# Performance work log

Measured on AMD Instinct MI355X. Metric: run time of the kernel, lower is better.

The kernel has to match this reference:

```python
import jax, jax.numpy as jnp
import numpy as np

HID = 768; HEADS = 12; DH = 64; W = 256  # one-sided window (attention_window=512)
L = 2; VOCAB = 50265; FFN = 3072; NLAB = 8921; B = 2; S = 4096
NEG = -1e9


def _ln(x, s, b):
    m = x.mean(-1, keepdims=True)
    v = ((x - m) ** 2).mean(-1, keepdims=True)
    return (x - m) * jax.lax.rsqrt(v + 1e-5) * s + b


def setup_inputs() -> dict:
    key = jax.random.key(0)
    ks = iter(jax.random.split(key, 64))
    def n(shape, sd=0.02):
        return jax.random.normal(next(ks), shape, jnp.float32) * sd
    inp = {
        'input_ids': jax.random.randint(next(ks), (B, S), 0, VOCAB, dtype=jnp.int32),
        'attention_mask': jnp.ones((B, S), jnp.int32),
        'word_emb': n((VOCAB, HID)), 'pos_emb': n((S, HID)),
        'emb_ln_s': jnp.ones((HID,), jnp.float32), 'emb_ln_b': jnp.zeros((HID,), jnp.float32),
        'Wq': n((L, HID, HID)), 'bq': jnp.zeros((L, HID), jnp.float32),
        'Wk': n((L, HID, HID)), 'bk': jnp.zeros((L, HID), jnp.float32),
        'Wv': n((L, HID, HID)), 'bv': jnp.zeros((L, HID), jnp.float32),
        'Wqg': n((L, HID, HID)), 'bqg': jnp.zeros((L, HID), jnp.float32),
        'Wkg': n((L, HID, HID)), 'bkg': jnp.zeros((L, HID), jnp.float32),
        'Wvg': n((L, HID, HID)), 'bvg': jnp.zeros((L, HID), jnp.float32),
        'Wo': n((L, HID, HID)), 'bo': jnp.zeros((L, HID), jnp.float32),
        'ln1_s': jnp.ones((L, HID), jnp.float32), 'ln1_b': jnp.zeros((L, HID), jnp.float32),
        'W1': n((L, HID, FFN)), 'b1': jnp.zeros((L, FFN), jnp.float32),
        'W2': n((L, FFN, HID)), 'b2': jnp.zeros((L, HID), jnp.float32),
        'ln2_s': jnp.ones((L, HID), jnp.float32), 'ln2_b': jnp.zeros((L, HID), jnp.float32),
        'head_W': n((HID, NLAB)), 'head_b': jnp.zeros((NLAB,), jnp.float32),
    }
    return inp


def _forward(input_ids, attention_mask, word_emb, pos_emb, emb_ln_s, emb_ln_b,
             Wq, bq, Wk, bk, Wv, bv, Wqg, bqg, Wkg, bkg, Wvg, bvg, Wo, bo,
             ln1_s, ln1_b, W1, b1, W2, b2, ln2_s, ln2_b, head_W, head_b):
    Bc, Sc = input_ids.shape
    nc = Sc // W
    scale = 1.0 / np.sqrt(DH).astype(np.float32)
    # embeddings
    x = word_emb[input_ids] + pos_emb[None, :Sc]
    x = _ln(x, emb_ln_s, emb_ln_b)
    # static band masks: query pos c*W+p, key pos (c-1)*W+kk in the 3-chunk layout
    p = jnp.arange(W)
    kk = jnp.arange(3 * W)
    rel = kk[None, :] - W - p[:, None]                     # [W,3W] key_pos - query_pos
    cpos = (jnp.arange(nc)[:, None, None] - 1) * W + kk[None, None, :]  # [nc,1,3W]
    valid = (cpos >= 0) & (cpos < Sc) & (cpos != 0) & (jnp.abs(rel)[None, :, :] <= W)  # [nc,W,3W]
    am_keys = attention_mask[:, jnp.clip(cpos, 0, Sc - 1)] > 0  # [B,nc,1,3W]
    band_mask = valid[None] & am_keys                        # [B,nc,W,3W]

    def split_heads(t):
        return t.reshape(Bc, Sc, HEADS, DH).transpose(0, 2, 1, 3)

    def chunk3(t):  # [B,H,S,D] -> [B,H,nc,3W,D] keys/values of chunks c-1,c,c+1
        tp = jnp.pad(t, ((0, 0), (0, 0), (W, W), (0, 0)))
        tr = tp.reshape(Bc, HEADS, nc + 2, W, DH)
        return jnp.concatenate([tr[:, :, :-2], tr[:, :, 1:-1], tr[:, :, 2:]], axis=3)

    for l in range(L):
        q = split_heads(x @ Wq[l] + bq[l])
        k = split_heads(x @ Wk[l] + bk[l])
        v = split_heads(x @ Wv[l] + bv[l])
        qg = split_heads(x @ Wqg[l] + bqg[l])
        kg = split_heads(x @ Wkg[l] + bkg[l])
        vg = split_heads(x @ Wvg[l] + bvg[l])
        # sliding-window banded scores
        qc = q.reshape(Bc, HEADS, nc, W, DH)
        kc = chunk3(k)
        vc = chunk3(v)
        sc = jnp.einsum('bhcqd,bhckd->bhcqk', qc, kc) * scale   # [B,H,nc,W,3W]
        sc = jnp.where(band_mask[:, None], sc, NEG)
        # extra column: every local query attends to the global (CLS) key
        g_col = jnp.einsum('bhsd,bhd->bhs', q, kg[:, :, 0]) * scale
        full = jnp.concatenate([g_col[..., None], sc.reshape(Bc, HEADS, Sc, 3 * W)], axis=-1)
        probs = jax.nn.softmax(full, axis=-1)
        p_g = probs[..., 0]
        p_b = probs[..., 1:].reshape(Bc, HEADS, nc, W, 3 * W)
        out = jnp.einsum('bhcqk,bhckd->bhcqd', p_b, vc).reshape(Bc, HEADS, Sc, DH)
        out = out + p_g[..., None] * vg[:, :, 0][:, :, None, :]
        # global (CLS) query: full attention over all tokens with global projections
        gs = jnp.einsum('bhd,bhsd->bhs', qg[:, :, 0], kg) * scale
        gs = jnp.where(attention_mask[:, None, :] > 0, gs, NEG)
        gp = jax.nn.softmax(gs, axis=-1)
        out0 = jnp.einsum('bhs,bhsd->bhd', gp, vg)
        out = out.at[:, :, 0, :].set(out0)
        # output proj + residual + LN, then FFN + residual + LN
        attn = out.transpose(0, 2, 1, 3).reshape(Bc, Sc, HID) @ Wo[l] + bo[l]
        x = _ln(x + attn, ln1_s[l], ln1_b[l])
        h = jax.nn.gelu(x @ W1[l] + b1[l], approximate=False) @ W2[l] + b2[l]
        x = _ln(x + h, ln2_s[l], ln2_b[l])
    # head on CLS token (dropout is identity in eval)
    return x[:, 0] @ head_W + head_b


def reference(input_ids, attention_mask, word_emb, pos_emb, emb_ln_s, emb_ln_b,
              Wq, bq, Wk, bk, Wv, bv, Wqg, bqg, Wkg, bkg, Wvg, bvg, Wo, bo,
              ln1_s, ln1_b, W1, b1, W2, b2, ln2_s, ln2_b, head_W, head_b):
    return _forward(input_ids, attention_mask, word_emb, pos_emb, emb_ln_s, emb_ln_b,
                    Wq, bq, Wk, bk, Wv, bv, Wqg, bqg, Wkg, bkg, Wvg, bvg, Wo, bo,
                    ln1_s, ln1_b, W1, b1, W2, b2, ln2_s, ln2_b, head_W, head_b)
```

## Files before the change

### kernel.cpp

```cpp
#include <hip/hip_runtime.h>
#include <hip/hip_bf16.h>
#include <math.h>

#define HIDN 768
#define NHEAD 12
#define DHEAD 64
#define WWIN 256
#define NCHUNK 16
#define NLAYER 2
#define FFND 3072
#define NLABEL 8921
#define NB 2
#define NS 4096
#define NBS (NB*NS)

#define QSTR 3840
#define OQ   0
#define OK_  768
#define OV   1536
#define OKG  2304
#define OVG  3072

typedef __attribute__((ext_vector_type(8))) short bf16x8;
typedef __attribute__((ext_vector_type(4))) float f32x4;

__device__ __forceinline__ float bf2f(unsigned short u){
  union { unsigned int i; float f; } v; v.i = ((unsigned int)u) << 16; return v.f;
}
__device__ __forceinline__ unsigned short f2bf(float f){
  __hip_bfloat16 h = __float2bfloat16(f);
  return *reinterpret_cast<unsigned short*>(&h);
}
__device__ __forceinline__ void unpack2(unsigned int u, float& a, float& b){
  union { unsigned int i; float f; } x, y;
  x.i = u << 16; y.i = u & 0xffff0000u; a = x.f; b = y.f;
}
__device__ __forceinline__ float gelu_f(float v){
  float x = v * 0.70710678118f;
  float ax = fabsf(x);
  float t = 1.0f / (1.0f + 0.3275911f*ax);
  float poly = ((((1.061405429f*t - 1.453152027f)*t + 1.421413741f)*t
                - 0.284496736f)*t + 0.254829592f)*t;
  float y = 1.0f - poly*__expf(-x*x);
  float er = copysignf(y, x);
  return 0.5f*v*(1.0f + er);
}
__device__ __forceinline__ void gld_lds16(const unsigned short* g, unsigned short* l){
  __builtin_amdgcn_global_load_lds((const __attribute__((address_space(1))) unsigned int*)g,
                                   (__attribute__((address_space(3))) unsigned int*)l, 16, 0, 0);
}

__device__ __forceinline__ int xcd_swz(int orig, int nwg){
  int q = nwg >> 3, r = nwg & 7;
  int x = orig & 7, lo = orig >> 3;
  return (x < r ? x*(q+1) : r*(q+1) + (x-r)*q) + lo;
}

#define DPP_ROR_F(x, N) __builtin_bit_cast(float, __builtin_amdgcn_update_dpp( \
    0, __builtin_bit_cast(int, (x)), 0x120 + (N), 0xf, 0xf, true))
__device__ __forceinline__ float rowmax16(float x){
  x = fmaxf(x, DPP_ROR_F(x, 1));
  x = fmaxf(x, DPP_ROR_F(x, 2));
  x = fmaxf(x, DPP_ROR_F(x, 4));
  x = fmaxf(x, DPP_ROR_F(x, 8));
  return x;
}
__device__ __forceinline__ float rowsum16(float x){
  x = x + DPP_ROR_F(x, 1);
  x = x + DPP_ROR_F(x, 2);
  x = x + DPP_ROR_F(x, 4);
  x = x + DPP_ROR_F(x, 8);
  return x;
}

__global__ __launch_bounds__(256) void embed_k(const int* __restrict__ ids,
    const float* __restrict__ we, const float* __restrict__ pe,
    float* __restrict__ y){
  int i = blockIdx.x*256 + threadIdx.x;
  int row = i / HIDN; int d = i - row*HIDN;
  int s = row & (NS-1);
  int id = ids[row];
  y[i] = we[(size_t)id*HIDN + d] + pe[(size_t)s*HIDN + d];
}

__global__ __launch_bounds__(256) void ln_k(const float* A, const float* R,
    const float* __restrict__ sc, const float* __restrict__ bi,
    float* X, unsigned short* XB){
  __shared__ float red[256];
  int row = blockIdx.x, t = threadIdx.x;
  size_t base = (size_t)row*HIDN;
  float v0 = A[base+t], v1 = A[base+t+256], v2 = A[base+t+512];
  if (R){ v0 += R[base+t]; v1 += R[base+t+256]; v2 += R[base+t+512]; }
  red[t] = v0+v1+v2; __syncthreads();
  for (int st=128; st>0; st>>=1){ if (t<st) red[t]+=red[t+st]; __syncthreads(); }
  float mean = red[0] * (1.0f/HIDN); __syncthreads();
  float d0=v0-mean, d1=v1-mean, d2=v2-mean;
  red[t] = d0*d0+d1*d1+d2*d2; __syncthreads();
  for (int st=128; st>0; st>>=1){ if (t<st) red[t]+=red[t+st]; __syncthreads(); }
  float rs = rsqrtf(red[0] * (1.0f/HIDN) + 1e-5f);
  float o0 = d0*rs*sc[t]     + bi[t];
  float o1 = d1*rs*sc[t+256] + bi[t+256];
  float o2 = d2*rs*sc[t+512] + bi[t+512];
  X[base+t]=o0; X[base+t+256]=o1; X[base+t+512]=o2;
  XB[base+t]=f2bf(o0); XB[base+t+256]=f2bf(o1); XB[base+t+512]=f2bf(o2);
}

__global__ __launch_bounds__(256) void transpose_k(const float* __restrict__ src,
    unsigned short* __restrict__ dst, int R, int C){
  __shared__ unsigned short tile[32][33];
  int ct = blockIdx.x*32, rt = blockIdx.y*32;
  int tx = threadIdx.x, ty = threadIdx.y;
  #pragma unroll
  for (int i=0;i<4;i++) tile[ty+i*8][tx] = f2bf(src[(size_t)(rt+ty+i*8)*C + ct + tx]);
  __syncthreads();
  #pragma unroll
  for (int i=0;i<4;i++) dst[(size_t)(ct+ty+i*8)*R + rt + tx] = tile[tx][ty+i*8];
}

__global__ __launch_bounds__(256) void pack_bias_k(const float* __restrict__ bq,
    const float* __restrict__ bk, const float* __restrict__ bv,
    const float* __restrict__ bkg, const float* __restrict__ bvg,
    float* __restrict__ out){
  int i = blockIdx.x*256 + threadIdx.x;
  int l = i / QSTR; int j = i - l*QSTR;
  int seg = j / HIDN, d = j - seg*HIDN;
  const float* src = (seg==0)?bq : (seg==1)?bk : (seg==2)?bv : (seg==3)?bkg : bvg;
  out[i] = src[l*HIDN + d];
}

template<int OUTF32, int GELU>
__global__ __launch_bounds__(256) void gemm128(const unsigned short* __restrict__ A,
    const unsigned short* __restrict__ BT, const float* __restrict__ bias,
    void* __restrict__ Cp, int M, int N, int K){
  __shared__ unsigned short As[128*64];
  __shared__ unsigned short Bs[128*64];
  const int tid = threadIdx.x;
  const int nwg = gridDim.x * gridDim.y;
  const int wg = xcd_swz(blockIdx.y * gridDim.x + blockIdx.x, nwg);
  const int m0 = (wg / gridDim.x) * 128, n0 = (wg % gridDim.x) * 128;
  const int lane = tid & 63, w = tid >> 6;
  const int n = lane & 15, quad = lane >> 4;
  const int wm = (w>>1)*64, wn = (w&1)*64;
  const int lr = lane >> 3, site = lane & 7;
  f32x4 acc[4][4] = {};
  for (int kb=0; kb<K; kb+=64){
    #pragma unroll
    for (int j=0;j<4;j++){
      int rbase = w*32 + j*8;
      int r = rbase + lr;
      int q = site ^ (r & 7);
      gld_lds16(A  + (size_t)(m0+r)*K + kb + q*8, &As[rbase*64]);
      gld_lds16(BT + (size_t)(n0+r)*K + kb + q*8, &Bs[rbase*64]);
    }
    __syncthreads();
    #pragma unroll
    for (int ks=0; ks<2; ks++){
      bf16x8 a[4], b[4];
      #pragma unroll
      for (int i=0;i<4;i++){
        int rm = wm + i*16 + n;
        a[i] = *(const bf16x8*)&As[rm*64 + (((ks*4+quad) ^ (rm&7))<<3)];
        int rn = wn + i*16 + n;
        b[i] = *(const bf16x8*)&Bs[rn*64 + (((ks*4+quad) ^ (rn&7))<<3)];
      }
      #pragma unroll
      for (int mi=0;mi<4;mi++)
      #pragma unroll
      for (int ni=0;ni<4;ni++)
        acc[mi][ni] = __builtin_amdgcn_mfma_f32_16x16x32_bf16(a[mi], b[ni], acc[mi][ni], 0,0,0);
    }
    __syncthreads();
  }
  #pragma unroll
  for (int mi=0; mi<4; mi++)
  #pragma unroll
  for (int ni=0; ni<4; ni++){
    int col = n0 + wn + ni*16 + n;
    float bsv = bias[col];
    #pragma unroll
    for (int rg=0; rg<4; rg++){
      int row = m0 + wm + mi*16 + quad*4 + rg;
      float v = acc[mi][ni][rg] + bsv;
      if (GELU) v = gelu_f(v);
      if (OUTF32) ((float*)Cp)[(size_t)row*N + col] = v;
      else ((unsigned short*)Cp)[(size_t)row*N + col] = f2bf(v);
    }
  }
}

template<int OUTF32, int GELU>
__global__ __launch_bounds__(512) void gemm256(const unsigned short* __restrict__ A,
    const unsigned short* __restrict__ BT, const float* __restrict__ bias,
    void* __restrict__ Cp, int M, int N, int K){
  __shared__ unsigned short AsB[2][256*64];
  __shared__ unsigned short BsB[2][256*64];
  const int tid = threadIdx.x;
  const int gx = gridDim.x;
  const int nwg = gx * gridDim.y;
  const int wg = xcd_swz(blockIdx.y*gx + blockIdx.x, nwg);
  const int m0 = (wg / gx) * 256, n0 = (wg % gx) * 256;
  const int lane = tid & 63, w = tid >> 6;
  const int n = lane & 15, quad = lane >> 4;
  const int wm = (w>>2)*128, wn = (w&3)*64;
  const int lr = lane >> 3, site = lane & 7;
  const int NK = K >> 6;
  f32x4 acc[8][4] = {};

  auto stage = [&](int b, int kb){
    #pragma unroll
    for (int j=0;j<4;j++){
      int rbase = w*32 + j*8;
      int r = rbase + lr;
      int q = site ^ (r & 7);
      gld_lds16(A  + (size_t)(m0+r)*K + kb + q*8, &AsB[b][rbase*64]);
      gld_lds16(BT + (size_t)(n0+r)*K + kb + q*8, &BsB[b][rbase*64]);
    }
  };

  stage(0, 0);
  asm volatile("s_waitcnt vmcnt(0)" ::: "memory");
  __builtin_amdgcn_s_barrier();

  int cur = 0;
  for (int kt=0; kt<NK; ++kt){
    if (kt+1 < NK) stage(cur^1, (kt+1)<<6);
    const unsigned short* As_ = AsB[cur];
    const unsigned short* Bs_ = BsB[cur];
    bf16x8 bfr[2][4];
    #pragma unroll
    for (int ks=0;ks<2;ks++)
    #pragma unroll
    for (int ni=0;ni<4;ni++){
      int rn = wn + ni*16 + n;
      bfr[ks][ni] = *(const bf16x8*)&Bs_[rn*64 + (((ks*4+quad) ^ (rn&7))<<3)];
    }
    #pragma unroll
    for (int mi=0;mi<8;mi++){
      int rm = wm + mi*16 + n;
      bf16x8 a0 = *(const bf16x8*)&As_[rm*64 + (((quad)     ^ (rm&7))<<3)];
      bf16x8 a1 = *(const bf16x8*)&As_[rm*64 + (((4+quad)   ^ (rm&7))<<3)];
      #pragma unroll
      for (int ni=0;ni<4;ni++)
        acc[mi][ni] = __builtin_amdgcn_mfma_f32_16x16x32_bf16(a0, bfr[0][ni], acc[mi][ni],0,0,0);
      #pragma unroll
      for (int ni=0;ni<4;ni++)
        acc[mi][ni] = __builtin_amdgcn_mfma_f32_16x16x32_bf16(a1, bfr[1][ni], acc[mi][ni],0,0,0);
    }
    if (kt+1 < NK){
      asm volatile("s_waitcnt vmcnt(0)" ::: "memory");
      __builtin_amdgcn_s_barrier();
    }
    cur ^= 1;
  }
  #pragma unroll
  for (int mi=0;mi<8;mi++)
  #pragma unroll
  for (int ni=0;ni<4;ni++){
    int col = n0 + wn + ni*16 + n;
    float bsv = bias[col];
    #pragma unroll
    for (int rg=0;rg<4;rg++){
      int row = m0 + wm + mi*16 + quad*4 + rg;
      float v = acc[mi][ni][rg] + bsv;
      if (GELU) v = gelu_f(v);
      if (OUTF32) ((float*)Cp)[(size_t)row*N + col] = v;
      else ((unsigned short*)Cp)[(size_t)row*N + col] = f2bf(v);
    }
  }
}

__global__ __launch_bounds__(256, 2) void band_attn_mfma(
    const unsigned short* __restrict__ qkv, const int* __restrict__ am,
    unsigned short* __restrict__ Out){
  __shared__ unsigned short Kt[64*72];
  __shared__ unsigned short Vt[64*72];
  __shared__ unsigned short Pbuf[4*64*72];
  __shared__ float mk[64];
  __shared__ unsigned short kgs[64];
  __shared__ unsigned short vgs[64];

  const int tid = threadIdx.x;
  const int bid = xcd_swz(blockIdx.x, gridDim.x);
  const int c = bid & (NCHUNK-1);
  const int h = (bid / NCHUNK) % NHEAD;
  const int b = bid / (NCHUNK*NHEAD);
  const int lane = tid & 63, w = tid >> 6;
  const int n = lane & 15, quad = lane >> 4;
  const int qbase = w * 64;
  unsigned short* Pw = Pbuf + w*64*72;

  if (tid < 8)       ((uint4*)kgs)[tid]   = ((const uint4*)(qkv + ((size_t)b*NS)*QSTR + OKG + h*DHEAD))[tid];
  else if (tid < 16) ((uint4*)vgs)[tid-8] = ((const uint4*)(qkv + ((size_t)b*NS)*QSTR + OVG + h*DHEAD))[tid-8];
  __syncthreads();

  bf16x8 aQ[4][2];
  #pragma unroll
  for (int mi=0; mi<4; mi++)
  #pragma unroll
  for (int ks=0; ks<2; ks++)
    aQ[mi][ks] = *(const bf16x8*)(qkv + ((size_t)(b*NS + c*WWIN + qbase + 16*mi + n))*QSTR
                                    + OQ + h*DHEAD + ks*32 + quad*8);

  f32x4 sacc[4] = {};
  #pragma unroll
  for (int ks=0; ks<2; ks++){
    bf16x8 bg = *(const bf16x8*)(kgs + ks*32 + quad*8);
    bf16x8 z8 = {};
    bg = (n == 0) ? bg : z8;
    #pragma unroll
    for (int mi=0; mi<4; mi++)
      sacc[mi] = __builtin_amdgcn_mfma_f32_16x16x32_bf16(aQ[mi][ks], bg, sacc[mi], 0,0,0);
  }
  float mst[4][4], lpt[4][4];
  f32x4 apv[4][4];
  float vgf[4];
  #pragma unroll
  for (int ni=0; ni<4; ni++) vgf[ni] = bf2f(vgs[16*ni + n]);
  #pragma unroll
  for (int mi=0; mi<4; mi++)
  #pragma unroll
  for (int rg=0; rg<4; rg++){
    float sg = __shfl(sacc[mi][rg], lane & 48);
    mst[mi][rg] = sg * 0.125f;
    lpt[mi][rg] = (n == 0) ? 1.0f : 0.0f;
  }
  #pragma unroll
  for (int mi=0; mi<4; mi++)
  #pragma unroll
  for (int ni=0; ni<4; ni++)
  #pragma unroll
  for (int rg=0; rg<4; rg++) apv[mi][ni][rg] = vgf[ni];

  for (int t=0; t<12; t++){
    __syncthreads();
    {
      int i = tid >> 2, d0 = (tid & 3) * 8;
      int kp = (c-1)*WWIN + t*64 + i;
      int kpc = min(max(kp, 0), NS-1);
      size_t gb = ((size_t)(b*NS + kpc))*QSTR + h*DHEAD;
      uint4 k0 = *(const uint4*)(qkv + gb + OK_ + d0);
      uint4 k1 = *(const uint4*)(qkv + gb + OK_ + d0 + 32);
      uint4 v0 = *(const uint4*)(qkv + gb + OV + d0);
      uint4 v1 = *(const uint4*)(qkv + gb + OV + d0 + 32);
      *(uint4*)(Kt + i*72 + d0) = k0;
      *(uint4*)(Kt + i*72 + d0 + 32) = k1;
      const unsigned short* s0 = (const unsigned short*)&v0;
      const unsigned short* s1 = (const unsigned short*)&v1;
      #pragma unroll
      for (int j=0;j<8;j++){
        Vt[(d0+j)*72 + i] = s0[j];
        Vt[(d0+32+j)*72 + i] = s1[j];
      }
      if ((tid & 3) == 0)
        mk[i] = (kp >= 1 && kp < NS && am[b*NS + kpc] > 0) ? 0.0f : -1e9f;
    }
    __syncthreads();

    float mkv[4];
    #pragma unroll
    for (int ni=0; ni<4; ni++) mkv[ni] = mk[16*ni + n];

    f32x4 accs[4][4] = {};
    #pragma unroll
    for (int ks=0; ks<2; ks++){
      bf16x8 bK[4];
      #pragma unroll
      for (int ni=0; ni<4; ni++)
        bK[ni] = *(const bf16x8*)(Kt + (16*ni + n)*72 + ks*32 + quad*8);
      #pragma unroll
      for (int mi=0; mi<4; mi++)
      #pragma unroll
      for (int ni=0; ni<4; ni++)
        accs[mi][ni] = __builtin_amdgcn_mfma_f32_16x16x32_bf16(aQ[mi][ks], bK[ni], accs[mi][ni], 0,0,0);
    }

    #pragma unroll
    for (int mi=0; mi<4; mi++){
      float sv[4][4];
      #pragma unroll
      for (int ni=0; ni<4; ni++)
      #pragma unroll
      for (int rg=0; rg<4; rg++){
        int kk = t*64 + 16*ni + n;
        int pr = qbase + 16*mi + quad*4 + rg;
        float s = accs[mi][ni][rg]*0.125f + mkv[ni];
        if ((unsigned)(kk - pr) > 512u) s = -1e9f;
        sv[ni][rg] = s;
      }
      #pragma unroll
      for (int rg=0; rg<4; rg++){
        float rm = fmaxf(fmaxf(sv[0][rg], sv[1][rg]), fmaxf(sv[2][rg], sv[3][rg]));
        rm = rowmax16(rm);
        float mold = mst[mi][rg];
        float mnew = fmaxf(mold, rm);
        float alpha = __expf(mold - mnew);
        mst[mi][rg] = mnew;
        float psum = 0.f;
        #pragma unroll
        for (int ni=0; ni<4; ni++){
          float pv = __expf(sv[ni][rg] - mnew);
          sv[ni][rg] = pv;
          psum += pv;
        }
        lpt[mi][rg] = lpt[mi][rg]*alpha + psum;
        #pragma unroll
        for (int ni=0; ni<4; ni++) apv[mi][ni][rg] *= alpha;
        int prow = 16*mi + quad*4 + rg;
        #pragma unroll
        for (int ni=0; ni<4; ni++)
          Pw[prow*72 + 16*ni + n] = f2bf(sv[ni][rg]);
      }
    }

    #pragma unroll
    for (int ks2=0; ks2<2; ks2++){
      bf16x8 aP[4], bV[4];
      #pragma unroll
      for (int mi=0; mi<4; mi++)
        aP[mi] = *(const bf16x8*)(Pw + (16*mi + n)*72 + ks2*32 + quad*8);
      #pragma unroll
      for (int ni=0; ni<4; ni++)
        bV[ni] = *(const bf16x8*)(Vt + (16*ni + n)*72 + ks2*32 + quad*8);
      #pragma unroll
      for (int mi=0; mi<4; mi++)
      #pragma unroll
      for (int ni=0; ni<4; ni++)
        apv[mi][ni] = __builtin_amdgcn_mfma_f32_16x16x32_bf16(aP[mi], bV[ni], apv[mi][ni], 0,0,0);
    }
  }

  #pragma unroll
  for (int mi=0; mi<4; mi++)
  #pragma unroll
  for (int rg=0; rg<4; rg++){
    float L = rowsum16(lpt[mi][rg]);
    float inv = 1.0f / L;
    int q = c*WWIN + qbase + 16*mi + quad*4 + rg;
    size_t ob = ((size_t)(b*NS + q))*HIDN + h*DHEAD;
    #pragma unroll
    for (int ni=0; ni<4; ni++)
      Out[ob + 16*ni + n] = f2bf(apv[mi][ni][rg] * inv);
  }
}

__global__ __launch_bounds__(128) void gattn_part(
    const unsigned short* __restrict__ QG0, const unsigned short* __restrict__ qkv,
    const int* __restrict__ am, float* __restrict__ part){
  __shared__ float qs[64];
  __shared__ float ps[128];
  __shared__ float red[128];
  int t = threadIdx.x;
  int cx = blockIdx.x, h = blockIdx.y, b = blockIdx.z;
  if (t < 32){
    float a, bb; unpack2(((const unsigned int*)(QG0 + (size_t)b*128*HIDN + h*DHEAD))[t], a, bb);
    qs[2*t]=a*0.125f; qs[2*t+1]=bb*0.125f;
  }
  __syncthreads();
  int kp = cx*128 + t;
  const unsigned int* kr = (const unsigned int*)(qkv + ((size_t)(b*NS+kp))*QSTR + OKG + h*DHEAD);
  float sv = 0.f;
  #pragma unroll
  for (int j=0;j<32;j++){ float a,bb; unpack2(kr[j],a,bb); sv += qs[2*j]*a + qs[2*j+1]*bb; }
  if (am[b*NS+kp] <= 0) sv = -1e9f;
  red[t] = sv; __syncthreads();
  for (int st=64; st>0; st>>=1){ if (t<st) red[t] = fmaxf(red[t], red[t+st]); __syncthreads(); }
  float M = red[0]; __syncthreads();
  float e = __expf(sv - M);
  ps[t] = e; red[t] = e; __syncthreads();
  for (int st=64; st>0; st>>=1){ if (t<st) red[t] += red[t+st]; __syncthreads(); }
  float L = red[0];
  float* po = part + ((size_t)((b*NHEAD+h)*32 + cx))*66;
  if (t==0){ po[0]=M; po[1]=L; }
  if (t < 64){
    float o = 0.f;
    #pragma unroll 4
    for (int i=0;i<128;i++)
      o += ps[i] * bf2f(qkv[((size_t)(b*NS + cx*128 + i))*QSTR + OVG + h*DHEAD + t]);
    po[2+t] = o;
  }
}

__global__ __launch_bounds__(64) void gattn_reduce(const float* __restrict__ part,
    unsigned short* __restrict__ Out){
  int bh = blockIdx.x;
  int b = bh / NHEAD, h = bh % NHEAD;
  int d = threadIdx.x;
  const float* pp = part + (size_t)bh*32*66;
  float M = -1e30f;
  for (int c2=0;c2<32;c2++) M = fmaxf(M, pp[c2*66]);
  float L = 0.f, o = 0.f;
  for (int c2=0;c2<32;c2++){
    float w = __expf(pp[c2*66] - M);
    L += pp[c2*66+1]*w;
    o += pp[c2*66+2+d]*w;
  }
  Out[((size_t)b*NS)*HIDN + h*DHEAD + d] = f2bf(o / L);
}

__global__ __launch_bounds__(256) void head_k(const float* __restrict__ X,
    const float* __restrict__ HW, const float* __restrict__ HB,
    float* __restrict__ Outp){
  __shared__ float red[256];
  __shared__ float xs[HIDN];
  int b = blockIdx.y;
  int base = blockIdx.x*64;
  int t = threadIdx.x;
  const float* x0 = X + (size_t)b*NS*HIDN;
  for (int i=t; i<HIDN; i+=256) xs[i] = x0[i];
  __syncthreads();
  int n = base + (t & 63);
  int dp = t >> 6;
  float a = 0.f;
  if (n < NLABEL){
    #pragma unroll 4
    for (int d=dp*192; d<dp*192+192; ++d)
      a += xs[d] * HW[(size_t)d*NLABEL + n];
  }
  red[t] = a; __syncthreads();
  if (t < 64 && n < NLABEL)
    Outp[(size_t)b*NLABEL + n] = red[t]+red[t+64]+red[t+128]+red[t+192] + HB[n];
}

extern "C" void kernel_launch(void* const* d_in, const int* in_sizes, int n_in,
                              void* d_out, int out_size, void* d_ws, size_t ws_size,
                              hipStream_t stream){
  (void)in_sizes; (void)n_in; (void)out_size; (void)ws_size;
  const int* ids = (const int*)d_in[0];
  const int* am  = (const int*)d_in[1];
  const float* we  = (const float*)d_in[2];
  const float* pe  = (const float*)d_in[3];
  const float* elns= (const float*)d_in[4];
  const float* elnb= (const float*)d_in[5];
  const float* Wq  = (const float*)d_in[6];
  const float* bq  = (const float*)d_in[7];
  const float* Wk  = (const float*)d_in[8];
  const float* bk  = (const float*)d_in[9];
  const float* Wv  = (const float*)d_in[10];
  const float* bv  = (const float*)d_in[11];
  const float* Wqg = (const float*)d_in[12];
  const float* bqg = (const float*)d_in[13];
  const float* Wkg = (const float*)d_in[14];
  const float* bkg = (const float*)d_in[15];
  const float* Wvg = (const float*)d_in[16];
  const float* bvg = (const float*)d_in[17];
  const float* Wo  = (const float*)d_in[18];
  const float* bo  = (const float*)d_in[19];
  const float* l1s = (const float*)d_in[20];
  const float* l1b = (const float*)d_in[21];
  const float* W1  = (const float*)d_in[22];
  const float* b1  = (const float*)d_in[23];
  const float* W2  = (const float*)d_in[24];
  const float* b2  = (const float*)d_in[25];
  const float* l2s = (const float*)d_in[26];
  const float* l2b = (const float*)d_in[27];
  const float* hW  = (const float*)d_in[28];
  const float* hB  = (const float*)d_in[29];

  char* ws = (char*)d_ws;
  float* x = (float*)ws;
  float* y = (float*)(ws + 25165824);
  unsigned short* xb   = (unsigned short*)(ws + 50331648);
  unsigned short* qkvb = (unsigned short*)(ws + 62914560);
  unsigned short* qg0b = (unsigned short*)(ws + 125829120);
  float* part = (float*)(ws + 126222336);
  unsigned short* ao   = (unsigned short*)(ws + 126425088);
  unsigned short* hbuf = (unsigned short*)(ws + 139008000);
  unsigned short* wt   = (unsigned short*)(ws + 189339648);
  float* bpack = (float*)(ws + 224729088);

  const size_t SQ = 589824;
  const size_t SW = 2359296;
  const size_t PERL = 7*SQ + 2*SW;

  auto tr = [&](const float* src, unsigned short* dst, int R, int C){
    dim3 g(C/32, R/32), blk(32, 8);
    transpose_k<<<g, blk, 0, stream>>>(src, dst, R, C);
  };
  for (int l=0; l<NLAYER; l++){
    unsigned short* base = wt + (size_t)l*PERL;
    tr(Wq  + (size_t)l*SQ, base + 0*SQ, 768, 768);
    tr(Wk  + (size_t)l*SQ, base + 1*SQ, 768, 768);
    tr(Wv  + (size_t)l*SQ, base + 2*SQ, 768, 768);
    tr(Wkg + (size_t)l*SQ, base + 3*SQ, 768, 768);
    tr(Wvg + (size_t)l*SQ, base + 4*SQ, 768, 768);
    tr(Wqg + (size_t)l*SQ, base + 5*SQ, 768, 768);
    tr(Wo  + (size_t)l*SQ, base + 6*SQ, 768, 768);
    tr(W1  + (size_t)l*SW, base + 7*SQ, 768, 3072);
    tr(W2  + (size_t)l*SW, base + 7*SQ + SW, 3072, 768);
  }
  pack_bias_k<<<(NLAYER*QSTR)/256, 256, 0, stream>>>(bq, bk, bv, bkg, bvg, bpack);

  embed_k<<<(NBS*HIDN)/256, 256, 0, stream>>>(ids, we, pe, y);
  ln_k<<<NBS, 256, 0, stream>>>(y, nullptr, elns, elnb, x, xb);

  for (int l=0; l<NLAYER; l++){
    unsigned short* base = wt + (size_t)l*PERL;
    gemm256<0,0><<<dim3(15,32), 512, 0, stream>>>(xb, base, bpack + (size_t)l*QSTR,
                                                  qkvb, NBS, QSTR, 768);
    for (int b=0; b<NB; b++)
      gemm128<0,0><<<dim3(6,1), 256, 0, stream>>>(xb + (size_t)b*NS*HIDN, base + 5*SQ,
                                                  bqg + l*768, qg0b + (size_t)b*128*HIDN,
                                                  128, 768, 768);
    band_attn_mfma<<<NB*NHEAD*NCHUNK, 256, 0, stream>>>(qkvb, am, ao);
    gattn_part<<<dim3(32, NHEAD, NB), 128, 0, stream>>>(qg0b, qkvb, am, part);
    gattn_reduce<<<NB*NHEAD, 64, 0, stream>>>(part, ao);
    gemm128<1,0><<<dim3(6,64), 256, 0, stream>>>(ao, base + 6*SQ, bo + l*768, y, NBS, 768, 768);
    ln_k<<<NBS, 256, 0, stream>>>(y, x, l1s + l*768, l1b + l*768, x, xb);
    gemm256<0,1><<<dim3(12,32), 512, 0, stream>>>(xb, base + 7*SQ, b1 + l*3072, hbuf, NBS, 3072, 768);
    gemm128<1,0><<<dim3(6,64), 256, 0, stream>>>(hbuf, base + 7*SQ + SW, b2 + l*768, y, NBS, 768, 3072);
    ln_k<<<NBS, 256, 0, stream>>>(y, x, l2s + l*768, l2b + l*768, x, xb);
  }

  head_k<<<dim3((NLABEL+63)/64, NB), 256, 0, stream>>>(x, hW, hB, (float*)d_out);
}
```

Baseline: 1.165 ms.

## Batch weight transposes into one launch, merge qg GEMMs, single-buffer gemm256

All 18 weight transpose launches are folded into one kernel that looks up its matrix from a block-offset table. The two per-batch global-query GEMM launches become one launch with a z-dimension. gemm256 drops its double-buffered LDS prefetch for a single buffer with __syncthreads and adds s_setprio around the MFMA loop. This cuts launch overhead and halves gemm256 LDS use, which may allow more occupancy, but it gives up overlap of global loads with compute in the largest GEMMs.

```diff
diff --git a/kernel.cpp b/kernel.cpp
--- a/kernel.cpp
+++ b/kernel.cpp
@@ -105,10 +105,24 @@
   XB[base+t]=f2bf(o0); XB[base+t+256]=f2bf(o1); XB[base+t+512]=f2bf(o2);
 }
 
-__global__ __launch_bounds__(256) void transpose_k(const float* __restrict__ src,
-    unsigned short* __restrict__ dst, int R, int C){
+struct TrTable {
+  const float* src[18];
+  unsigned short* dst[18];
+  int R[18]; int C[18];
+  int t0[19];
+};
+__global__ __launch_bounds__(256) void transpose_all_k(TrTable tt){
   __shared__ unsigned short tile[32][33];
-  int ct = blockIdx.x*32, rt = blockIdx.y*32;
+  int bid = blockIdx.x;
+  int m = 0;
+  #pragma unroll 1
+  while (bid >= tt.t0[m+1]) m++;
+  int local = bid - tt.t0[m];
+  int C = tt.C[m], R = tt.R[m];
+  int Ct = C >> 5;
+  int ct = (local % Ct) * 32, rt = (local / Ct) * 32;
+  const float* src = tt.src[m];
+  unsigned short* dst = tt.dst[m];
   int tx = threadIdx.x, ty = threadIdx.y;
   #pragma unroll
   for (int i=0;i<4;i++) tile[ty+i*8][tx] = f2bf(src[(size_t)(rt+ty+i*8)*C + ct + tx]);
@@ -188,12 +202,69 @@
   }
 }
 
+__global__ __launch_bounds__(256) void gemm128qg(const unsigned short* __restrict__ A0,
+    const unsigned short* __restrict__ BT, const float* __restrict__ bias,
+    unsigned short* __restrict__ C0){
+  __shared__ unsigned short As[128*64];
+  __shared__ unsigned short Bs[128*64];
+  const unsigned short* A = A0 + (size_t)blockIdx.z*NS*HIDN;
+  unsigned short* C = C0 + (size_t)blockIdx.z*128*HIDN;
+  const int K = 768, N = 768;
+  const int tid = threadIdx.x;
+  const int n0 = blockIdx.x * 128;
+  const int lane = tid & 63, w = tid >> 6;
+  const int n = lane & 15, quad = lane >> 4;
+  const int wm = (w>>1)*64, wn = (w&1)*64;
+  const int lr = lane >> 3, site = lane & 7;
+  f32x4 acc[4][4] = {};
+  for (int kb=0; kb<K; kb+=64){
+    #pragma unroll
+    for (int j=0;j<4;j++){
+      int rbase = w*32 + j*8;
+      int r = rbase + lr;
+      int q = site ^ (r & 7);
+      gld_lds16(A  + (size_t)r*K + kb + q*8, &As[rbase*64]);
+      gld_lds16(BT + (size_t)(n0+r)*K + kb + q*8, &Bs[rbase*64]);
+    }
+    __syncthreads();
+    #pragma unroll
+    for (int ks=0; ks<2; ks++){
+      bf16x8 a[4], b[4];
+      #pragma unroll
+      for (int i=0;i<4;i++){
+        int rm = wm + i*16 + n;
+        a[i] = *(const bf16x8*)&As[rm*64 + (((ks*4+quad) ^ (rm&7))<<3)];
+        int rn = wn + i*16 + n;
+        b[i] = *(const bf16x8*)&Bs[rn*64 + (((ks*4+quad) ^ (rn&7))<<3)];
+      }
+      #pragma unroll
+      for (int mi=0;mi<4;mi++)
+      #pragma unroll
+      for (int ni=0;ni<4;ni++)
+        acc[mi][ni] = __builtin_amdgcn_mfma_f32_16x16x32_bf16(a[mi], b[ni], acc[mi][ni], 0,0,0);
+    }
+    __syncthreads();
+  }
+  #pragma unroll
+  for (int mi=0; mi<4; mi++)
+  #pragma unroll
+  for (int ni=0; ni<4; ni++){
+    int col = n0 + wn + ni*16 + n;
+    float bsv = bias[col];
+    #pragma unroll
+    for (int rg=0; rg<4; rg++){
+      int row = wm + mi*16 + quad*4 + rg;
+      C[(size_t)row*N + col] = f2bf(acc[mi][ni][rg] + bsv);
+    }
+  }
+}
+
 template<int OUTF32, int GELU>
 __global__ __launch_bounds__(512) void gemm256(const unsigned short* __restrict__ A,
     const unsigned short* __restrict__ BT, const float* __restrict__ bias,
     void* __restrict__ Cp, int M, int N, int K){
-  __shared__ unsigned short AsB[2][256*64];
-  __shared__ unsigned short BsB[2][256*64];
+  __shared__ unsigned short As[256*64];
+  __shared__ unsigned short Bs[256*64];
   const int tid = threadIdx.x;
   const int gx = gridDim.x;
   const int nwg = gx * gridDim.y;
@@ -203,42 +274,32 @@
   const int n = lane & 15, quad = lane >> 4;
   const int wm = (w>>2)*128, wn = (w&3)*64;
   const int lr = lane >> 3, site = lane & 7;
-  const int NK = K >> 6;
   f32x4 acc[8][4] = {};
 
-  auto stage = [&](int b, int kb){
+  for (int kb=0; kb<K; kb+=64){
     #pragma unroll
     for (int j=0;j<4;j++){
       int rbase = w*32 + j*8;
       int r = rbase + lr;
       int q = site ^ (r & 7);
-      gld_lds16(A  + (size_t)(m0+r)*K + kb + q*8, &AsB[b][rbase*64]);
-      gld_lds16(BT + (size_t)(n0+r)*K + kb + q*8, &BsB[b][rbase*64]);
-    }
-  };
-
-  stage(0, 0);
-  asm volatile("s_waitcnt vmcnt(0)" ::: "memory");
-  __builtin_amdgcn_s_barrier();
-
-  int cur = 0;
-  for (int kt=0; kt<NK; ++kt){
-    if (kt+1 < NK) stage(cur^1, (kt+1)<<6);
-    const unsigned short* As_ = AsB[cur];
-    const unsigned short* Bs_ = BsB[cur];
+      gld_lds16(A  + (size_t)(m0+r)*K + kb + q*8, &As[rbase*64]);
+      gld_lds16(BT + (size_t)(n0+r)*K + kb + q*8, &Bs[rbase*64]);
+    }
+    __syncthreads();
     bf16x8 bfr[2][4];
     #pragma unroll
     for (int ks=0;ks<2;ks++)
     #pragma unroll
     for (int ni=0;ni<4;ni++){
       int rn = wn + ni*16 + n;
-      bfr[ks][ni] = *(const bf16x8*)&Bs_[rn*64 + (((ks*4+quad) ^ (rn&7))<<3)];
-    }
+      bfr[ks][ni] = *(const bf16x8*)&Bs[rn*64 + (((ks*4+quad) ^ (rn&7))<<3)];
+    }
+    __builtin_amdgcn_s_setprio(1);
     #pragma unroll
     for (int mi=0;mi<8;mi++){
       int rm = wm + mi*16 + n;
-      bf16x8 a0 = *(const bf16x8*)&As_[rm*64 + (((quad)     ^ (rm&7))<<3)];
-      bf16x8 a1 = *(const bf16x8*)&As_[rm*64 + (((4+quad)   ^ (rm&7))<<3)];
+      bf16x8 a0 = *(const bf16x8*)&As[rm*64 + (((quad)     ^ (rm&7))<<3)];
+      bf16x8 a1 = *(const bf16x8*)&As[rm*64 + (((4+quad)   ^ (rm&7))<<3)];
       #pragma unroll
       for (int ni=0;ni<4;ni++)
         acc[mi][ni] = __builtin_amdgcn_mfma_f32_16x16x32_bf16(a0, bfr[0][ni], acc[mi][ni],0,0,0);
@@ -246,11 +307,8 @@
       for (int ni=0;ni<4;ni++)
         acc[mi][ni] = __builtin_amdgcn_mfma_f32_16x16x32_bf16(a1, bfr[1][ni], acc[mi][ni],0,0,0);
     }
-    if (kt+1 < NK){
-      asm volatile("s_waitcnt vmcnt(0)" ::: "memory");
-      __builtin_amdgcn_s_barrier();
-    }
-    cur ^= 1;
+    __builtin_amdgcn_s_setprio(0);
+    __syncthreads();
   }
   #pragma unroll
   for (int mi=0;mi<8;mi++)
@@ -572,22 +630,24 @@
   const size_t SW = 2359296;
   const size_t PERL = 7*SQ + 2*SW;
 
-  auto tr = [&](const float* src, unsigned short* dst, int R, int C){
-    dim3 g(C/32, R/32), blk(32, 8);
-    transpose_k<<<g, blk, 0, stream>>>(src, dst, R, C);
-  };
+  TrTable tt;
+  int nt = 0, tacc = 0;
   for (int l=0; l<NLAYER; l++){
     unsigned short* base = wt + (size_t)l*PERL;
-    tr(Wq  + (size_t)l*SQ, base + 0*SQ, 768, 768);
-    tr(Wk  + (size_t)l*SQ, base + 1*SQ, 768, 768);
-    tr(Wv  + (size_t)l*SQ, base + 2*SQ, 768, 768);
-    tr(Wkg + (size_t)l*SQ, base + 3*SQ, 768, 768);
-    tr(Wvg + (size_t)l*SQ, base + 4*SQ, 768, 768);
-    tr(Wqg + (size_t)l*SQ, base + 5*SQ, 768, 768);
-    tr(Wo  + (size_t)l*SQ, base + 6*SQ, 768, 768);
-    tr(W1  + (size_t)l*SW, base + 7*SQ, 768, 3072);
-    tr(W2  + (size_t)l*SW, base + 7*SQ + SW, 3072, 768);
-  }
+    const float* srcs[9] = {Wq + (size_t)l*SQ, Wk + (size_t)l*SQ, Wv + (size_t)l*SQ,
+                            Wkg + (size_t)l*SQ, Wvg + (size_t)l*SQ, Wqg + (size_t)l*SQ,
+                            Wo + (size_t)l*SQ, W1 + (size_t)l*SW, W2 + (size_t)l*SW};
+    unsigned short* dsts[9] = {base, base+SQ, base+2*SQ, base+3*SQ, base+4*SQ,
+                               base+5*SQ, base+6*SQ, base+7*SQ, base+7*SQ+SW};
+    int Rs[9] = {768,768,768,768,768,768,768,768,3072};
+    int Cs[9] = {768,768,768,768,768,768,768,3072,768};
+    for (int k=0;k<9;k++){
+      tt.src[nt]=srcs[k]; tt.dst[nt]=dsts[k]; tt.R[nt]=Rs[k]; tt.C[nt]=Cs[k];
+      tt.t0[nt]=tacc; tacc += (Rs[k]/32)*(Cs[k]/32); nt++;
+    }
+  }
+  tt.t0[18]=tacc;
+  transpose_all_k<<<tacc, dim3(32,8), 0, stream>>>(tt);
   pack_bias_k<<<(NLAYER*QSTR)/256, 256, 0, stream>>>(bq, bk, bv, bkg, bvg, bpack);
 
   embed_k<<<(NBS*HIDN)/256, 256, 0, stream>>>(ids, we, pe, y);
@@ -597,10 +657,7 @@
     unsigned short* base = wt + (size_t)l*PERL;
     gemm256<0,0><<<dim3(15,32), 512, 0, stream>>>(xb, base, bpack + (size_t)l*QSTR,
                                                   qkvb, NBS, QSTR, 768);
-    for (int b=0; b<NB; b++)
-      gemm128<0,0><<<dim3(6,1), 256, 0, stream>>>(xb + (size_t)b*NS*HIDN, base + 5*SQ,
-                                                  bqg + l*768, qg0b + (size_t)b*128*HIDN,
-                                                  128, 768, 768);
+    gemm128qg<<<dim3(6,1,2), 256, 0, stream>>>(xb, base + 5*SQ, bqg + l*768, qg0b);
     band_attn_mfma<<<NB*NHEAD*NCHUNK, 256, 0, stream>>>(qkvb, am, ao);
     gattn_part<<<dim3(32, NHEAD, NB), 128, 0, stream>>>(qg0b, qkvb, am, part);
     gattn_reduce<<<NB*NHEAD, 64, 0, stream>>>(part, ao);
```

Measured after the change: 1.121 ms. 1.04x faster.
